# Optimization experiments

Measured on AMD Instinct MI355X. Metric: run time of the kernel, lower is better.

The kernel has to match this reference:

```python
import jax, jax.numpy as jnp
import numpy as np

MAX_LENGTH = 13
PAD_TOKEN = 0
HIDDEN = 1024
VOCAB = 32000
BATCH = 64


def gru_cell(x, h, w_ih, w_hh, b_ih, b_hh):
    # PyTorch GRU gate order: reset, update, new
    gi = x @ w_ih.T + b_ih            # [B, 3H]
    gh = h @ w_hh.T + b_hh            # [B, 3H]
    i_r, i_z, i_n = jnp.split(gi, 3, axis=-1)
    h_r, h_z, h_n = jnp.split(gh, 3, axis=-1)
    r = jax.nn.sigmoid(i_r + h_r)
    z = jax.nn.sigmoid(i_z + h_z)
    n = jnp.tanh(i_n + r * h_n)
    return (1.0 - z) * n + z * h


def setup_inputs() -> dict:
    key = jax.random.key(0)
    ks = jax.random.split(key, 9)
    s = 0.02
    return {
        "encoder_outputs": jax.random.normal(ks[0], (BATCH, MAX_LENGTH, HIDDEN), jnp.float32),
        "encoder_hidden": jax.random.normal(ks[1], (1, BATCH, HIDDEN), jnp.float32),
        "embedding": jax.random.normal(ks[2], (VOCAB, HIDDEN), jnp.float32) * s,
        "w_ih": jax.random.normal(ks[3], (3 * HIDDEN, HIDDEN), jnp.float32) * s,
        "w_hh": jax.random.normal(ks[4], (3 * HIDDEN, HIDDEN), jnp.float32) * s,
        "b_ih": jnp.zeros((3 * HIDDEN,), jnp.float32),
        "b_hh": jnp.zeros((3 * HIDDEN,), jnp.float32),
        "w_out": jax.random.normal(ks[5], (VOCAB, HIDDEN), jnp.float32) * s,
        "b_out": jnp.zeros((VOCAB,), jnp.float32),
    }


def reference(encoder_outputs, encoder_hidden, embedding, w_ih, w_hh, b_ih, b_hh, w_out, b_out):
    batch = encoder_outputs.shape[0]
    h0 = encoder_hidden[0]                               # [B, H]
    tok0 = jnp.full((batch,), PAD_TOKEN, dtype=jnp.int32)

    def step(carry, _):
        h, tok = carry
        x = jax.nn.relu(embedding[tok])                  # embed + relu
        h = gru_cell(x, h, w_ih, w_hh, b_ih, b_hh)       # GRU cell
        logits = h @ w_out.T + b_out                     # [B, V]
        nxt = jnp.argmax(logits, axis=-1).astype(jnp.int32)  # greedy feedback (topk(1))
        return (h, nxt), logits

    (h_final, _), logits = jax.lax.scan(step, (h0, tok0), None, length=MAX_LENGTH)
    logits = jnp.transpose(logits, (1, 0, 2))            # [B, T, V]
    log_probs = jax.nn.log_softmax(logits, axis=-1)
    return log_probs, h_final[None]
```

## Files before the change

### kernel.cpp

```cpp
#include <hip/hip_runtime.h>
#include <math.h>

#define BB 64
#define HH 1024
#define VV 32000
#define TT 13
#define QS 8000
#define BKL 128

typedef float f32x4 __attribute__((ext_vector_type(4)));
typedef __bf16 bf16x8 __attribute__((ext_vector_type(8)));

__device__ __forceinline__ unsigned short f2bf(float f) {
  unsigned u = __float_as_uint(f);
  u = (u + 0x7fffu + ((u >> 16) & 1u)) >> 16;
  return (unsigned short)u;
}
__device__ __forceinline__ float bf2f(unsigned short s) {
  return __uint_as_float(((unsigned)s) << 16);
}

__device__ __forceinline__ void gld16(const void* g, void* l) {
  __builtin_amdgcn_global_load_lds(
      (const __attribute__((address_space(1))) unsigned int*)g,
      (__attribute__((address_space(3))) unsigned int*)l, 16, 0, 0);
}

__global__ __launch_bounds__(1024) void k_init(
    const float* __restrict__ enc, const float* __restrict__ emb,
    float* __restrict__ hrm, unsigned short* __restrict__ hhi,
    unsigned short* __restrict__ hlo, unsigned short* __restrict__ xhi,
    unsigned short* __restrict__ xlo) {
  const int g = blockIdx.x * 1024 + threadIdx.x;
  const float h = enc[g];
  hrm[g] = h;
  const unsigned short h16 = f2bf(h);
  hhi[g] = h16;
  hlo[g] = f2bf(h - bf2f(h16));
  float e = emb[threadIdx.x];
  e = e > 0.f ? e : 0.f;
  const unsigned short e16 = f2bf(e);
  xhi[g] = e16;
  xlo[g] = f2bf(e - bf2f(e16));
}

__global__ __launch_bounds__(256) void k_wconv(const float* __restrict__ w,
                                               unsigned short* __restrict__ o) {
  const int n4 = VV * HH / 4;
  for (int i = blockIdx.x * 256 + threadIdx.x; i < n4; i += gridDim.x * 256) {
    const f32x4 v = ((const f32x4*)w)[i];
    ushort4 u;
    u.x = f2bf(v[0]); u.y = f2bf(v[1]); u.z = f2bf(v[2]); u.w = f2bf(v[3]);
    ((ushort4*)o)[i] = u;
  }
}

__global__ __launch_bounds__(256) void k_wconv2(
    const float* __restrict__ wih, const float* __restrict__ whh,
    unsigned short* __restrict__ ghi, unsigned short* __restrict__ glo) {
  const int n4 = 6 * HH * HH / 4;
  for (int i = blockIdx.x * 256 + threadIdx.x; i < n4; i += gridDim.x * 256) {
    const int flat = i * 4;
    const float* src = flat < 3 * HH * HH ? wih + flat : whh + (flat - 3 * HH * HH);
    const f32x4 v = *(const f32x4*)src;
    ushort4 hi, lo;
    hi.x = f2bf(v[0]); lo.x = f2bf(v[0] - bf2f(hi.x));
    hi.y = f2bf(v[1]); lo.y = f2bf(v[1] - bf2f(hi.y));
    hi.z = f2bf(v[2]); lo.z = f2bf(v[2] - bf2f(hi.z));
    hi.w = f2bf(v[3]); lo.w = f2bf(v[3] - bf2f(hi.w));
    ((ushort4*)ghi)[i] = hi;
    ((ushort4*)glo)[i] = lo;
  }
}

__global__ __launch_bounds__(64) void k_gru(
    const unsigned short* __restrict__ xhi, const unsigned short* __restrict__ xlo,
    const unsigned short* __restrict__ hhi_s, const unsigned short* __restrict__ hlo_s,
    const unsigned short* __restrict__ ghi, const unsigned short* __restrict__ glo,
    const float* __restrict__ wih, const float* __restrict__ whh,
    float* __restrict__ gbuf, int cachegw) {
  const int blk = blockIdx.x, lane = threadIdx.x;
  const int kh = blk & 1;
  const int r2 = blk >> 1;
  const int g6 = r2 % 6, jt = r2 / 6;
  const unsigned short* Ahi = g6 < 3 ? xhi : hhi_s;
  const unsigned short* Alo = g6 < 3 ? xlo : hlo_s;
  const int cl = lane & 15, kk = (lane >> 4) * 8;
  const int j = jt * 16 + cl;
  const int kbeg = kh * 512;
  f32x4 acc[4];
  acc[0] = acc[1] = acc[2] = acc[3] = (f32x4){0.f, 0.f, 0.f, 0.f};

  if (cachegw) {
    const unsigned short* bh = ghi + (size_t)(g6 * HH + j) * HH + kbeg;
    const unsigned short* bl = glo + (size_t)(g6 * HH + j) * HH + kbeg;
    const unsigned short* ah = Ahi + kbeg;
    const unsigned short* al = Alo + kbeg;
    #pragma unroll 4
    for (int k0 = 0; k0 < 512; k0 += 32) {
      const bf16x8 whi = *(const bf16x8*)(bh + k0 + kk);
      const bf16x8 wlo = *(const bf16x8*)(bl + k0 + kk);
      #pragma unroll
      for (int rt = 0; rt < 4; ++rt) {
        const size_t aoff = (size_t)(rt * 16 + cl) * HH + k0 + kk;
        const bf16x8 a_h = *(const bf16x8*)(ah + aoff);
        const bf16x8 a_l = *(const bf16x8*)(al + aoff);
        acc[rt] = __builtin_amdgcn_mfma_f32_16x16x32_bf16(a_h, whi, acc[rt], 0, 0, 0);
        acc[rt] = __builtin_amdgcn_mfma_f32_16x16x32_bf16(a_l, whi, acc[rt], 0, 0, 0);
        acc[rt] = __builtin_amdgcn_mfma_f32_16x16x32_bf16(a_h, wlo, acc[rt], 0, 0, 0);
      }
    }
  } else {
    const float* W = (g6 < 3 ? wih : whh) + (size_t)((g6 % 3) * HH + j) * HH + kbeg;
    for (int k0 = 0; k0 < 512; k0 += 32) {
      const f32x4 w0 = *(const f32x4*)(W + k0 + kk);
      const f32x4 w1 = *(const f32x4*)(W + k0 + kk + 4);
      union { unsigned short u[8]; bf16x8 b; } chi, clo;
      #pragma unroll
      for (int u2 = 0; u2 < 4; ++u2) {
        chi.u[u2] = f2bf(w0[u2]); clo.u[u2] = f2bf(w0[u2] - bf2f(chi.u[u2]));
        chi.u[4 + u2] = f2bf(w1[u2]); clo.u[4 + u2] = f2bf(w1[u2] - bf2f(chi.u[4 + u2]));
      }
      #pragma unroll
      for (int rt = 0; rt < 4; ++rt) {
        const size_t aoff = (size_t)(rt * 16 + cl) * HH + kbeg + k0 + kk;
        const bf16x8 a_h = *(const bf16x8*)(Ahi + aoff);
        const bf16x8 a_l = *(const bf16x8*)(Alo + aoff);
        acc[rt] = __builtin_amdgcn_mfma_f32_16x16x32_bf16(a_h, chi.b, acc[rt], 0, 0, 0);
        acc[rt] = __builtin_amdgcn_mfma_f32_16x16x32_bf16(a_l, chi.b, acc[rt], 0, 0, 0);
        acc[rt] = __builtin_amdgcn_mfma_f32_16x16x32_bf16(a_h, clo.b, acc[rt], 0, 0, 0);
      }
    }
  }
  #pragma unroll
  for (int rt = 0; rt < 4; ++rt)
    #pragma unroll
    for (int rg = 0; rg < 4; ++rg) {
      const int row = rt * 16 + (lane >> 4) * 4 + rg;
      gbuf[(size_t)((kh * 6 + g6) * BB + row) * HH + jt * 16 + cl] = acc[rt][rg];
    }
}

__global__ __launch_bounds__(256) void k_gep(
    const float* __restrict__ gbuf, const float* __restrict__ bih,
    const float* __restrict__ bhh, const float* __restrict__ hsrc,
    float* __restrict__ hdst, unsigned short* __restrict__ hhi_d,
    unsigned short* __restrict__ hlo_d) {
  const int e = blockIdx.x * 256 + threadIdx.x;
  const int b = e >> 10, j = e & (HH - 1);
  const size_t base = (size_t)b * HH + j;
  const float gir = gbuf[(size_t)(0 * BB + b) * HH + j] + gbuf[(size_t)((6 + 0) * BB + b) * HH + j] + bih[j];
  const float giz = gbuf[(size_t)(1 * BB + b) * HH + j] + gbuf[(size_t)((6 + 1) * BB + b) * HH + j] + bih[HH + j];
  const float gin = gbuf[(size_t)(2 * BB + b) * HH + j] + gbuf[(size_t)((6 + 2) * BB + b) * HH + j] + bih[2 * HH + j];
  const float ghr = gbuf[(size_t)(3 * BB + b) * HH + j] + gbuf[(size_t)((6 + 3) * BB + b) * HH + j] + bhh[j];
  const float ghz = gbuf[(size_t)(4 * BB + b) * HH + j] + gbuf[(size_t)((6 + 4) * BB + b) * HH + j] + bhh[HH + j];
  const float ghn = gbuf[(size_t)(5 * BB + b) * HH + j] + gbuf[(size_t)((6 + 5) * BB + b) * HH + j] + bhh[2 * HH + j];
  const float r_ = 1.f / (1.f + __expf(-(gir + ghr)));
  const float z_ = 1.f / (1.f + __expf(-(giz + ghz)));
  const float n_ = tanhf(gin + r_ * ghn);
  const float hnew = (1.f - z_) * n_ + z_ * hsrc[base];
  hdst[base] = hnew;
  const unsigned short h16 = f2bf(hnew);
  hhi_d[base] = h16;
  hlo_d[base] = f2bf(hnew - bf2f(h16));
}

__global__ __launch_bounds__(512, 1) void k_logits_lds(
    const unsigned short* __restrict__ hb,
    const unsigned short* __restrict__ wbf,
    const float* __restrict__ bout, float* __restrict__ lbuf) {
  __shared__ __attribute__((aligned(16))) unsigned char sA[2][64 * BKL * 2];
  __shared__ __attribute__((aligned(16))) unsigned char sB[2][128 * BKL * 2];
  const int tid = threadIdx.x, blk = blockIdx.x;
  const int lane = tid & 63, wv = tid >> 6;
  const int cl = lane & 15, kk = (lane >> 4) * 8;

  auto STAGE = [&](int buf, int k0) {
    #pragma unroll
    for (int it = 0; it < 2; ++it) {
      const int c = it * 512 + tid;
      const int r = c >> 4;
      const int kb = (c & 15) * 16;
      const int kbs = kb ^ ((r & 7) << 4);
      gld16(hb + (size_t)r * HH + k0 + (kbs >> 1),
            &sA[buf][it * 8192 + wv * 1024]);
    }
    #pragma unroll
    for (int it = 0; it < 4; ++it) {
      const int c = it * 512 + tid;
      const int col = c >> 4;
      const int kb = (c & 15) * 16;
      const int kbs = kb ^ ((col & 7) << 4);
      gld16(wbf + (size_t)(blk * 128 + col) * HH + k0 + (kbs >> 1),
            &sB[buf][it * 8192 + wv * 1024]);
    }
  };

  f32x4 acc[4];
  acc[0] = acc[1] = acc[2] = acc[3] = (f32x4){0.f, 0.f, 0.f, 0.f};

  STAGE(0, 0);
  for (int t = 0; t < HH / BKL; ++t) {
    const int cur = t & 1;
    if (t < HH / BKL - 1) {
      STAGE(cur ^ 1, (t + 1) * BKL);
      asm volatile("s_waitcnt vmcnt(6)" ::: "memory");
    } else {
      asm volatile("s_waitcnt vmcnt(0)" ::: "memory");
    }
    __builtin_amdgcn_s_barrier();
    __builtin_amdgcn_sched_barrier(0);
    #pragma unroll
    for (int ks = 0; ks < BKL; ks += 32) {
      const int bc = wv * 16 + cl;
      const bf16x8 bfr = *(const bf16x8*)&sB[cur][bc * (BKL * 2) + (((ks + kk) * 2) ^ ((bc & 7) << 4))];
      #pragma unroll
      for (int rt = 0; rt < 4; ++rt) {
        const int ar = rt * 16 + cl;
        const bf16x8 afr = *(const bf16x8*)&sA[cur][ar * (BKL * 2) + (((ks + kk) * 2) ^ ((ar & 7) << 4))];
        acc[rt] = __builtin_amdgcn_mfma_f32_16x16x32_bf16(afr, bfr, acc[rt], 0, 0, 0);
      }
    }
    __builtin_amdgcn_s_barrier();
    __builtin_amdgcn_sched_barrier(0);
  }

  const int col = blk * 128 + wv * 16 + cl;
  const float bo = bout[col];
  #pragma unroll
  for (int rt = 0; rt < 4; ++rt)
    #pragma unroll
    for (int rg = 0; rg < 4; ++rg) {
      const int row = rt * 16 + (lane >> 4) * 4 + rg;
      lbuf[(size_t)row * VV + col] = acc[rt][rg] + bo;
    }
}

__global__ __launch_bounds__(256) void k_logits_fb(
    const unsigned short* __restrict__ hb, const float* __restrict__ wout,
    const float* __restrict__ bout, float* __restrict__ lbuf) {
  const int tid = threadIdx.x, blk = blockIdx.x;
  const int lane = tid & 63, wv = tid >> 6;
  const int n0 = blk * 64 + wv * 16;
  const int cl = lane & 15, kk = (lane >> 4) * 8;
  f32x4 acc[4];
  acc[0] = acc[1] = acc[2] = acc[3] = (f32x4){0.f, 0.f, 0.f, 0.f};
  const float* wrow = wout + (size_t)(n0 + cl) * HH;
  for (int k0 = 0; k0 < HH; k0 += 32) {
    const f32x4 w0 = *(const f32x4*)(wrow + k0 + kk);
    const f32x4 w1 = *(const f32x4*)(wrow + k0 + kk + 4);
    union { unsigned short u[8]; bf16x8 b; } cv;
    #pragma unroll
    for (int u2 = 0; u2 < 4; ++u2) { cv.u[u2] = f2bf(w0[u2]); cv.u[4 + u2] = f2bf(w1[u2]); }
    #pragma unroll
    for (int rt = 0; rt < 4; ++rt) {
      const bf16x8 afr = *(const bf16x8*)(hb + (size_t)(rt * 16 + cl) * HH + k0 + kk);
      acc[rt] = __builtin_amdgcn_mfma_f32_16x16x32_bf16(afr, cv.b, acc[rt], 0, 0, 0);
    }
  }
  const int col = n0 + cl;
  const float bo = bout[col];
  #pragma unroll
  for (int rt = 0; rt < 4; ++rt)
    #pragma unroll
    for (int rg = 0; rg < 4; ++rg) {
      const int row = rt * 16 + (lane >> 4) * 4 + rg;
      lbuf[(size_t)row * VV + col] = acc[rt][rg] + bo;
    }
}

__global__ __launch_bounds__(256) void k_sum(
    const float* __restrict__ lbuf, const float* __restrict__ wout,
    const float* __restrict__ bout, const float* __restrict__ hnew,
    float* __restrict__ mq, float* __restrict__ sq,
    float* __restrict__ qbestV, int* __restrict__ qbestI, int dorecheck) {
  __shared__ float srow[QS];
  __shared__ float red[4];
  __shared__ int icnt;
  __shared__ int scand[32];
  const int tid = threadIdx.x;
  const int b = blockIdx.x >> 2, q = blockIdx.x & 3;
  const int lane = tid & 63, wv = tid >> 6;
  const f32x4* src = (const f32x4*)(lbuf + (size_t)b * VV + q * QS);
  f32x4* s4 = (f32x4*)srow;

  float m = -3.0e38f;
  for (int i = tid; i < QS / 4; i += 256) {
    const f32x4 v = src[i];
    s4[i] = v;
    m = fmaxf(fmaxf(fmaxf(m, v[0]), v[1]), fmaxf(v[2], v[3]));
  }
  #pragma unroll
  for (int d = 1; d < 64; d <<= 1) m = fmaxf(m, __shfl_xor(m, d, 64));
  if (lane == 0) red[wv] = m;
  if (tid == 0) icnt = 0;
  __syncthreads();
  const float M = fmaxf(fmaxf(red[0], red[1]), fmaxf(red[2], red[3]));

  float s = 0.f;
  for (int i = tid; i < QS / 4; i += 256) {
    const f32x4 v = s4[i];
    s += __expf(v[0] - M) + __expf(v[1] - M) + __expf(v[2] - M) + __expf(v[3] - M);
  }
  #pragma unroll
  for (int d = 1; d < 64; d <<= 1) s += __shfl_xor(s, d, 64);
  __syncthreads();
  if (lane == 0) red[wv] = s;
  __syncthreads();
  if (tid == 0) {
    mq[b * 4 + q] = M;
    sq[b * 4 + q] = red[0] + red[1] + red[2] + red[3];
  }

  if (dorecheck) {
    const float thr = M - 0.05f;
    for (int i = tid; i < QS / 4; i += 256) {
      const f32x4 v = s4[i];
      #pragma unroll
      for (int u = 0; u < 4; ++u)
        if (v[u] >= thr) {
          const int c = atomicAdd(&icnt, 1);
          if (c < 32) scand[c] = q * QS + 4 * i + u;
        }
    }
    __syncthreads();
    if (wv == 0) {
      const int nc = icnt < 32 ? icnt : 32;
      const float* hrow = hnew + (size_t)b * HH;
      f32x4 h4[4];
      #pragma unroll
      for (int u = 0; u < 4; ++u) h4[u] = *(const f32x4*)(hrow + lane * 16 + u * 4);
      float best = -3.0e38f; int bi = 0x7fffffff;
      for (int ci = 0; ci < nc; ++ci) {
        const int v = scand[ci];
        const float* wrow = wout + (size_t)v * HH + lane * 16;
        float ss = 0.f;
        #pragma unroll
        for (int u = 0; u < 4; ++u) {
          const f32x4 w4 = *(const f32x4*)(wrow + u * 4);
          ss += h4[u][0] * w4[0] + h4[u][1] * w4[1] + h4[u][2] * w4[2] + h4[u][3] * w4[3];
        }
        #pragma unroll
        for (int d = 1; d < 64; d <<= 1) ss += __shfl_xor(ss, d, 64);
        ss += bout[v];
        if (ss > best || (ss == best && v < bi)) { best = ss; bi = v; }
      }
      if (lane == 0) { qbestV[b * 4 + q] = best; qbestI[b * 4 + q] = bi; }
    }
  }
}

__global__ __launch_bounds__(256) void k_out(
    const float* __restrict__ lbuf, const float* __restrict__ mq,
    const float* __restrict__ sq, const float* __restrict__ qbestV,
    const int* __restrict__ qbestI, const float* __restrict__ emb,
    const float* __restrict__ hnew, float* __restrict__ out,
    unsigned short* __restrict__ xhi, unsigned short* __restrict__ xlo, int t) {
  __shared__ int stok;
  const int tid = threadIdx.x;
  const int b = blockIdx.x >> 2, q = blockIdx.x & 3;

  const float m0 = mq[b * 4 + 0], m1 = mq[b * 4 + 1];
  const float m2 = mq[b * 4 + 2], m3 = mq[b * 4 + 3];
  const float Mg = fmaxf(fmaxf(m0, m1), fmaxf(m2, m3));
  const float Sg = sq[b * 4 + 0] * __expf(m0 - Mg) + sq[b * 4 + 1] * __expf(m1 - Mg) +
                   sq[b * 4 + 2] * __expf(m2 - Mg) + sq[b * 4 + 3] * __expf(m3 - Mg);
  const float LZ = Mg + logf(Sg);

  const f32x4* src = (const f32x4*)(lbuf + (size_t)b * VV + q * QS);
  f32x4* dst = (f32x4*)(out + ((size_t)b * TT + t) * VV + q * QS);
  for (int i = tid; i < QS / 4; i += 256)
    dst[i] = src[i] - LZ;

  if (q == 0 && t < TT - 1) {
    if (tid == 0) {
      float bv = qbestV[b * 4 + 0]; int bi = qbestI[b * 4 + 0];
      #pragma unroll
      for (int qq = 1; qq < 4; ++qq) {
        const float v = qbestV[b * 4 + qq]; const int i2 = qbestI[b * 4 + qq];
        if (v > bv || (v == bv && i2 < bi)) { bv = v; bi = i2; }
      }
      stok = bi;
    }
    __syncthreads();
    const int tok = stok;
    for (int j = tid; j < HH; j += 256) {
      float e = emb[(size_t)tok * HH + j];
      e = e > 0.f ? e : 0.f;
      const unsigned short e16 = f2bf(e);
      xhi[(size_t)b * HH + j] = e16;
      xlo[(size_t)b * HH + j] = f2bf(e - bf2f(e16));
    }
  }
  if (q == 0 && t == TT - 1) {
    for (int j = tid; j < HH; j += 256)
      out[(size_t)BB * TT * VV + (size_t)b * HH + j] = hnew[(size_t)b * HH + j];
  }
}

extern "C" void kernel_launch(void* const* d_in, const int* in_sizes, int n_in,
                              void* d_out, int out_size, void* d_ws, size_t ws_size,
                              hipStream_t stream) {
  const float* enc  = (const float*)d_in[1];
  const float* emb  = (const float*)d_in[2];
  const float* wih  = (const float*)d_in[3];
  const float* whh  = (const float*)d_in[4];
  const float* bih  = (const float*)d_in[5];
  const float* bhh  = (const float*)d_in[6];
  const float* wout = (const float*)d_in[7];
  const float* bout = (const float*)d_in[8];
  float* out = (float*)d_out;

  char* ws = (char*)d_ws;
  size_t off = 0;
  auto alloc = [&](size_t bytes) -> char* {
    char* p = ws + off;
    off += (bytes + 255) & ~(size_t)255;
    return p;
  };
  float* hrm = (float*)alloc((size_t)2 * BB * HH * 4);
  unsigned short* hhi = (unsigned short*)alloc((size_t)2 * BB * HH * 2);
  unsigned short* hlo = (unsigned short*)alloc((size_t)2 * BB * HH * 2);
  unsigned short* xhi = (unsigned short*)alloc((size_t)BB * HH * 2);
  unsigned short* xlo = (unsigned short*)alloc((size_t)BB * HH * 2);
  float* gbuf = (float*)alloc((size_t)12 * BB * HH * 4);
  float* lbuf = (float*)alloc((size_t)BB * VV * 4);
  float* mq = (float*)alloc((size_t)BB * 4 * 4);
  float* sq = (float*)alloc((size_t)BB * 4 * 4);
  float* qbestV = (float*)alloc((size_t)BB * 4 * 4);
  int* qbestI = (int*)alloc((size_t)BB * 4 * 4);
  unsigned short* wbf = (unsigned short*)alloc((size_t)VV * HH * 2);
  const int cachew = (ws_size >= off) ? 1 : 0;
  unsigned short* ghi = (unsigned short*)alloc((size_t)6 * HH * HH * 2);
  unsigned short* glo = (unsigned short*)alloc((size_t)6 * HH * HH * 2);
  const int cachegw = (ws_size >= off) ? 1 : 0;

  hipLaunchKernelGGL(k_init, dim3(64), dim3(1024), 0, stream,
                     enc, emb, hrm, hhi, hlo, xhi, xlo);
  if (cachew)
    hipLaunchKernelGGL(k_wconv, dim3(2048), dim3(256), 0, stream, wout, wbf);
  if (cachegw)
    hipLaunchKernelGGL(k_wconv2, dim3(1024), dim3(256), 0, stream, wih, whh, ghi, glo);

  for (int t = 0; t < TT; ++t) {
    const int p = t & 1;
    const float* hsrc = hrm + (size_t)p * BB * HH;
    float* hdst = hrm + (size_t)(p ^ 1) * BB * HH;
    const unsigned short* hhs = hhi + (size_t)p * BB * HH;
    const unsigned short* hls = hlo + (size_t)p * BB * HH;
    unsigned short* hhd = hhi + (size_t)(p ^ 1) * BB * HH;
    unsigned short* hld = hlo + (size_t)(p ^ 1) * BB * HH;

    hipLaunchKernelGGL(k_gru, dim3(768), dim3(64), 0, stream,
                       xhi, xlo, hhs, hls, ghi, glo, wih, whh, gbuf, cachegw);
    hipLaunchKernelGGL(k_gep, dim3(256), dim3(256), 0, stream,
                       gbuf, bih, bhh, hsrc, hdst, hhd, hld);
    if (cachew)
      hipLaunchKernelGGL(k_logits_lds, dim3(250), dim3(512), 0, stream,
                         hhd, wbf, bout, lbuf);
    else
      hipLaunchKernelGGL(k_logits_fb, dim3(500), dim3(256), 0, stream,
                         hhd, wout, bout, lbuf);
    hipLaunchKernelGGL(k_sum, dim3(256), dim3(256), 0, stream,
                       lbuf, wout, bout, hdst, mq, sq, qbestV, qbestI,
                       (t < TT - 1) ? 1 : 0);
    hipLaunchKernelGGL(k_out, dim3(256), dim3(256), 0, stream,
                       lbuf, mq, sq, qbestV, qbestI, emb, hdst, out, xhi, xlo, t);
  }
}
```

Before: 927.0 us.

## Fuse GRU gemm with gate epilogue and merge per-step softmax/argmax kernels

Replaces the split-K GRU gemm plus separate gate-epilogue kernel with one kernel. Each block computes all six gate projections for 4 hidden columns across 6 waves over the full K, then applies the GRU nonlinearity from shared memory. It also merges the two-kernel log-softmax/argmax-recheck/output path into one 64-block, 1024-thread kernel per batch row. This cuts launches and the global gbuf round trip, but the GRU MFMAs now keep only 4 of 16 output columns, wasting 3/4 of the compute, and the reduction uses only 64 blocks.

New measurement: 1.538 ms. +65.9%, slower.

```diff
diff --git a/kernel.cpp b/kernel.cpp
--- a/kernel.cpp
+++ b/kernel.cpp
@@ -73,12 +73,245 @@
   }
 }
 
-__global__ __launch_bounds__(64) void k_gru(
+__global__ __launch_bounds__(384, 1) void k_gruE(
     const unsigned short* __restrict__ xhi, const unsigned short* __restrict__ xlo,
     const unsigned short* __restrict__ hhi_s, const unsigned short* __restrict__ hlo_s,
     const unsigned short* __restrict__ ghi, const unsigned short* __restrict__ glo,
+    const float* __restrict__ bih, const float* __restrict__ bhh,
+    const float* __restrict__ hsrc, float* __restrict__ hdst,
+    unsigned short* __restrict__ hhi_d, unsigned short* __restrict__ hlo_d) {
+  __shared__ float g[6][64][9];
+  const int blk = blockIdx.x, tid = threadIdx.x;
+  const int lane = tid & 63, wv = tid >> 6;
+  const int cl = lane & 15, kk = (lane >> 4) * 8;
+  {
+    const int g6 = wv;
+    const unsigned short* Ahi = g6 < 3 ? xhi : hhi_s;
+    const unsigned short* Alo = g6 < 3 ? xlo : hlo_s;
+    const int col = blk * 4 + (cl & 3);
+    const unsigned short* bh = ghi + (size_t)(g6 * HH + col) * HH;
+    const unsigned short* bl = glo + (size_t)(g6 * HH + col) * HH;
+    f32x4 acc[4];
+    acc[0] = acc[1] = acc[2] = acc[3] = (f32x4){0.f, 0.f, 0.f, 0.f};
+    #pragma unroll 4
+    for (int k0 = 0; k0 < HH; k0 += 32) {
+      const bf16x8 whi = *(const bf16x8*)(bh + k0 + kk);
+      const bf16x8 wlo = *(const bf16x8*)(bl + k0 + kk);
+      #pragma unroll
+      for (int rt = 0; rt < 4; ++rt) {
+        const size_t aoff = (size_t)(rt * 16 + cl) * HH + k0 + kk;
+        const bf16x8 a_h = *(const bf16x8*)(Ahi + aoff);
+        const bf16x8 a_l = *(const bf16x8*)(Alo + aoff);
+        acc[rt] = __builtin_amdgcn_mfma_f32_16x16x32_bf16(a_h, whi, acc[rt], 0, 0, 0);
+        acc[rt] = __builtin_amdgcn_mfma_f32_16x16x32_bf16(a_l, whi, acc[rt], 0, 0, 0);
+        acc[rt] = __builtin_amdgcn_mfma_f32_16x16x32_bf16(a_h, wlo, acc[rt], 0, 0, 0);
+      }
+    }
+    if (cl < 4) {
+      #pragma unroll
+      for (int rt = 0; rt < 4; ++rt)
+        #pragma unroll
+        for (int rg = 0; rg < 4; ++rg)
+          g[g6][rt * 16 + (lane >> 4) * 4 + rg][cl] = acc[rt][rg];
+    }
+  }
+  __syncthreads();
+  if (tid < 256) {
+    const int c = tid & 3, b = tid >> 2;
+    const int j = blk * 4 + c;
+    const size_t base = (size_t)b * HH + j;
+    const float gir = g[0][b][c] + bih[j];
+    const float giz = g[1][b][c] + bih[HH + j];
+    const float gin = g[2][b][c] + bih[2 * HH + j];
+    const float ghr = g[3][b][c] + bhh[j];
+    const float ghz = g[4][b][c] + bhh[HH + j];
+    const float ghn = g[5][b][c] + bhh[2 * HH + j];
+    const float r_ = 1.f / (1.f + __expf(-(gir + ghr)));
+    const float z_ = 1.f / (1.f + __expf(-(giz + ghz)));
+    const float n_ = tanhf(gin + r_ * ghn);
+    const float hnew = (1.f - z_) * n_ + z_ * hsrc[base];
+    hdst[base] = hnew;
+    const unsigned short h16 = f2bf(hnew);
+    hhi_d[base] = h16;
+    hlo_d[base] = f2bf(hnew - bf2f(h16));
+  }
+}
+
+__global__ __launch_bounds__(512, 1) void k_logits_lds(
+    const unsigned short* __restrict__ hb,
+    const unsigned short* __restrict__ wbf,
+    const float* __restrict__ bout, float* __restrict__ lbuf) {
+  __shared__ __attribute__((aligned(16))) unsigned char sA[2][64 * BKL * 2];
+  __shared__ __attribute__((aligned(16))) unsigned char sB[2][128 * BKL * 2];
+  const int tid = threadIdx.x, blk = blockIdx.x;
+  const int lane = tid & 63, wv = tid >> 6;
+  const int cl = lane & 15, kk = (lane >> 4) * 8;
+
+  auto STAGE = [&](int buf, int k0) {
+    #pragma unroll
+    for (int it = 0; it < 2; ++it) {
+      const int c = it * 512 + tid;
+      const int r = c >> 4;
+      const int kb = (c & 15) * 16;
+      const int kbs = kb ^ ((r & 7) << 4);
+      gld16(hb + (size_t)r * HH + k0 + (kbs >> 1),
+            &sA[buf][it * 8192 + wv * 1024]);
+    }
+    #pragma unroll
+    for (int it = 0; it < 4; ++it) {
+      const int c = it * 512 + tid;
+      const int col = c >> 4;
+      const int kb = (c & 15) * 16;
+      const int kbs = kb ^ ((col & 7) << 4);
+      gld16(wbf + (size_t)(blk * 128 + col) * HH + k0 + (kbs >> 1),
+            &sB[buf][it * 8192 + wv * 1024]);
+    }
+  };
+
+  f32x4 acc[4];
+  acc[0] = acc[1] = acc[2] = acc[3] = (f32x4){0.f, 0.f, 0.f, 0.f};
+
+  STAGE(0, 0);
+  for (int t = 0; t < HH / BKL; ++t) {
+    const int cur = t & 1;
+    if (t < HH / BKL - 1) {
+      STAGE(cur ^ 1, (t + 1) * BKL);
+      asm volatile("s_waitcnt vmcnt(6)" ::: "memory");
+    } else {
+      asm volatile("s_waitcnt vmcnt(0)" ::: "memory");
+    }
+    __builtin_amdgcn_s_barrier();
+    __builtin_amdgcn_sched_barrier(0);
+    #pragma unroll
+    for (int ks = 0; ks < BKL; ks += 32) {
+      const int bc = wv * 16 + cl;
+      const bf16x8 bfr = *(const bf16x8*)&sB[cur][bc * (BKL * 2) + (((ks + kk) * 2) ^ ((bc & 7) << 4))];
+      #pragma unroll
+      for (int rt = 0; rt < 4; ++rt) {
+        const int ar = rt * 16 + cl;
+        const bf16x8 afr = *(const bf16x8*)&sA[cur][ar * (BKL * 2) + (((ks + kk) * 2) ^ ((ar & 7) << 4))];
+        acc[rt] = __builtin_amdgcn_mfma_f32_16x16x32_bf16(afr, bfr, acc[rt], 0, 0, 0);
+      }
+    }
+    __builtin_amdgcn_s_barrier();
+    __builtin_amdgcn_sched_barrier(0);
+  }
+
+  const int col = blk * 128 + wv * 16 + cl;
+  const float bo = bout[col];
+  #pragma unroll
+  for (int rt = 0; rt < 4; ++rt)
+    #pragma unroll
+    for (int rg = 0; rg < 4; ++rg) {
+      const int row = rt * 16 + (lane >> 4) * 4 + rg;
+      lbuf[(size_t)row * VV + col] = acc[rt][rg] + bo;
+    }
+}
+
+__global__ __launch_bounds__(1024, 1) void k_red(
+    const float* __restrict__ lbuf, const float* __restrict__ wout,
+    const float* __restrict__ bout, const float* __restrict__ emb,
+    const float* __restrict__ hnew, float* __restrict__ out,
+    unsigned short* __restrict__ xhi, unsigned short* __restrict__ xlo, int t) {
+  __shared__ struct {
+    float srow[VV];
+    float red[16];
+    int icnt, stok;
+    int scand[64];
+  } sm;
+  const int tid = threadIdx.x, b = blockIdx.x;
+  const int lane = tid & 63, wv = tid >> 6;
+  const f32x4* src = (const f32x4*)(lbuf + (size_t)b * VV);
+  f32x4* s4 = (f32x4*)sm.srow;
+
+  float m = -3.0e38f;
+  for (int i = tid; i < VV / 4; i += 1024) {
+    const f32x4 v = src[i];
+    s4[i] = v;
+    m = fmaxf(fmaxf(fmaxf(m, v[0]), v[1]), fmaxf(v[2], v[3]));
+  }
+  #pragma unroll
+  for (int d = 1; d < 64; d <<= 1) m = fmaxf(m, __shfl_xor(m, d, 64));
+  if (lane == 0) sm.red[wv] = m;
+  if (tid == 0) sm.icnt = 0;
+  __syncthreads();
+  float M = sm.red[0];
+  #pragma unroll
+  for (int w = 1; w < 16; ++w) M = fmaxf(M, sm.red[w]);
+
+  float s = 0.f;
+  for (int i = tid; i < VV / 4; i += 1024) {
+    const f32x4 v = s4[i];
+    s += __expf(v[0] - M) + __expf(v[1] - M) + __expf(v[2] - M) + __expf(v[3] - M);
+  }
+  #pragma unroll
+  for (int d = 1; d < 64; d <<= 1) s += __shfl_xor(s, d, 64);
+  __syncthreads();
+  if (lane == 0) sm.red[wv] = s;
+  __syncthreads();
+  float S = sm.red[0];
+  #pragma unroll
+  for (int w = 1; w < 16; ++w) S += sm.red[w];
+  const float LZ = M + logf(S);
+
+  if (t < TT - 1) {
+    const float thr = M - 0.05f;
+    for (int i = tid; i < VV / 4; i += 1024) {
+      const f32x4 v = s4[i];
+      #pragma unroll
+      for (int u = 0; u < 4; ++u)
+        if (v[u] >= thr) {
+          const int c = atomicAdd(&sm.icnt, 1);
+          if (c < 64) sm.scand[c] = 4 * i + u;
+        }
+    }
+    __syncthreads();
+    if (wv == 0) {
+      const int nc = sm.icnt < 64 ? sm.icnt : 64;
+      const float* hrow = hnew + (size_t)b * HH;
+      f32x4 h4[4];
+      #pragma unroll
+      for (int u = 0; u < 4; ++u) h4[u] = *(const f32x4*)(hrow + lane * 16 + u * 4);
+      float best = -3.0e38f; int bi = 0x7fffffff;
+      for (int ci = 0; ci < nc; ++ci) {
+        const int v = sm.scand[ci];
+        const float* wrow = wout + (size_t)v * HH + lane * 16;
+        float ss = 0.f;
+        #pragma unroll
+        for (int u = 0; u < 4; ++u) {
+          const f32x4 w4 = *(const f32x4*)(wrow + u * 4);
+          ss += h4[u][0] * w4[0] + h4[u][1] * w4[1] + h4[u][2] * w4[2] + h4[u][3] * w4[3];
+        }
+        #pragma unroll
+        for (int d = 1; d < 64; d <<= 1) ss += __shfl_xor(ss, d, 64);
+        ss += bout[v];
+        if (ss > best || (ss == best && v < bi)) { best = ss; bi = v; }
+      }
+      if (lane == 0) sm.stok = bi;
+    }
+    __syncthreads();
+    const int tok = sm.stok;
+    {
+      float e = emb[(size_t)tok * HH + tid];
+      e = e > 0.f ? e : 0.f;
+      const unsigned short e16 = f2bf(e);
+      xhi[(size_t)b * HH + tid] = e16;
+      xlo[(size_t)b * HH + tid] = f2bf(e - bf2f(e16));
+    }
+  }
+
+  f32x4* dst = (f32x4*)(out + ((size_t)b * TT + t) * VV);
+  for (int i = tid; i < VV / 4; i += 1024)
+    dst[i] = s4[i] - LZ;
+  if (t == TT - 1)
+    out[(size_t)BB * TT * VV + (size_t)b * HH + tid] = hnew[(size_t)b * HH + tid];
+}
+
+__global__ __launch_bounds__(64) void k_gru_fb(
+    const unsigned short* __restrict__ xhi, const unsigned short* __restrict__ xlo,
+    const unsigned short* __restrict__ hhi_s, const unsigned short* __restrict__ hlo_s,
     const float* __restrict__ wih, const float* __restrict__ whh,
-    float* __restrict__ gbuf, int cachegw) {
+    float* __restrict__ gbuf) {
   const int blk = blockIdx.x, lane = threadIdx.x;
   const int kh = blk & 1;
   const int r2 = blk >> 1;
@@ -90,46 +323,24 @@
   const int kbeg = kh * 512;
   f32x4 acc[4];
   acc[0] = acc[1] = acc[2] = acc[3] = (f32x4){0.f, 0.f, 0.f, 0.f};
-
-  if (cachegw) {
-    const unsigned short* bh = ghi + (size_t)(g6 * HH + j) * HH + kbeg;
-    const unsigned short* bl = glo + (size_t)(g6 * HH + j) * HH + kbeg;
-    const unsigned short* ah = Ahi + kbeg;
-    const unsigned short* al = Alo + kbeg;
-    #pragma unroll 4
-    for (int k0 = 0; k0 < 512; k0 += 32) {
-      const bf16x8 whi = *(const bf16x8*)(bh + k0 + kk);
-      const bf16x8 wlo = *(const bf16x8*)(bl + k0 + kk);
-      #pragma unroll
-      for (int rt = 0; rt < 4; ++rt) {
-        const size_t aoff = (size_t)(rt * 16 + cl) * HH + k0 + kk;
-        const bf16x8 a_h = *(const bf16x8*)(ah + aoff);
-        const bf16x8 a_l = *(const bf16x8*)(al + aoff);
-        acc[rt] = __builtin_amdgcn_mfma_f32_16x16x32_bf16(a_h, whi, acc[rt], 0, 0, 0);
-        acc[rt] = __builtin_amdgcn_mfma_f32_16x16x32_bf16(a_l, whi, acc[rt], 0, 0, 0);
-        acc[rt] = __builtin_amdgcn_mfma_f32_16x16x32_bf16(a_h, wlo, acc[rt], 0, 0, 0);
-      }
-    }
-  } else {
-    const float* W = (g6 < 3 ? wih : whh) + (size_t)((g6 % 3) * HH + j) * HH + kbeg;
-    for (int k0 = 0; k0 < 512; k0 += 32) {
-      const f32x4 w0 = *(const f32x4*)(W + k0 + kk);
-      const f32x4 w1 = *(const f32x4*)(W + k0 + kk + 4);
-      union { unsigned short u[8]; bf16x8 b; } chi, clo;
-      #pragma unroll
-      for (int u2 = 0; u2 < 4; ++u2) {
-        chi.u[u2] = f2bf(w0[u2]); clo.u[u2] = f2bf(w0[u2] - bf2f(chi.u[u2]));
-        chi.u[4 + u2] = f2bf(w1[u2]); clo.u[4 + u2] = f2bf(w1[u2] - bf2f(chi.u[4 + u2]));
-      }
-      #pragma unroll
-      for (int rt = 0; rt < 4; ++rt) {
-        const size_t aoff = (size_t)(rt * 16 + cl) * HH + kbeg + k0 + kk;
-        const bf16x8 a_h = *(const bf16x8*)(Ahi + aoff);
-        const bf16x8 a_l = *(const bf16x8*)(Alo + aoff);
-        acc[rt] = __builtin_amdgcn_mfma_f32_16x16x32_bf16(a_h, chi.b, acc[rt], 0, 0, 0);
-        acc[rt] = __builtin_amdgcn_mfma_f32_16x16x32_bf16(a_l, chi.b, acc[rt], 0, 0, 0);
-        acc[rt] = __builtin_amdgcn_mfma_f32_16x16x32_bf16(a_h, clo.b, acc[rt], 0, 0, 0);
-      }
+  const float* W = (g6 < 3 ? wih : whh) + (size_t)((g6 % 3) * HH + j) * HH + kbeg;
+  for (int k0 = 0; k0 < 512; k0 += 32) {
+    const f32x4 w0 = *(const f32x4*)(W + k0 + kk);
+    const f32x4 w1 = *(const f32x4*)(W + k0 + kk + 4);
+    union { unsigned short u[8]; bf16x8 b; } chi, clo;
+    #pragma unroll
+    for (int u2 = 0; u2 < 4; ++u2) {
+      chi.u[u2] = f2bf(w0[u2]); clo.u[u2] = f2bf(w0[u2] - bf2f(chi.u[u2]));
+      chi.u[4 + u2] = f2bf(w1[u2]); clo.u[4 + u2] = f2bf(w1[u2] - bf2f(chi.u[4 + u2]));
+    }
+    #pragma unroll
+    for (int rt = 0; rt < 4; ++rt) {
+      const size_t aoff = (size_t)(rt * 16 + cl) * HH + kbeg + k0 + kk;
+      const bf16x8 a_h = *(const bf16x8*)(Ahi + aoff);
+      const bf16x8 a_l = *(const bf16x8*)(Alo + aoff);
+      acc[rt] = __builtin_amdgcn_mfma_f32_16x16x32_bf16(a_h, chi.b, acc[rt], 0, 0, 0);
+      acc[rt] = __builtin_amdgcn_mfma_f32_16x16x32_bf16(a_l, chi.b, acc[rt], 0, 0, 0);
+      acc[rt] = __builtin_amdgcn_mfma_f32_16x16x32_bf16(a_h, clo.b, acc[rt], 0, 0, 0);
     }
   }
   #pragma unroll
@@ -165,77 +376,6 @@
   hlo_d[base] = f2bf(hnew - bf2f(h16));
 }
 
-__global__ __launch_bounds__(512, 1) void k_logits_lds(
-    const unsigned short* __restrict__ hb,
-    const unsigned short* __restrict__ wbf,
-    const float* __restrict__ bout, float* __restrict__ lbuf) {
-  __shared__ __attribute__((aligned(16))) unsigned char sA[2][64 * BKL * 2];
-  __shared__ __attribute__((aligned(16))) unsigned char sB[2][128 * BKL * 2];
-  const int tid = threadIdx.x, blk = blockIdx.x;
-  const int lane = tid & 63, wv = tid >> 6;
-  const int cl = lane & 15, kk = (lane >> 4) * 8;
-
-  auto STAGE = [&](int buf, int k0) {
-    #pragma unroll
-    for (int it = 0; it < 2; ++it) {
-      const int c = it * 512 + tid;
-      const int r = c >> 4;
-      const int kb = (c & 15) * 16;
-      const int kbs = kb ^ ((r & 7) << 4);
-      gld16(hb + (size_t)r * HH + k0 + (kbs >> 1),
-            &sA[buf][it * 8192 + wv * 1024]);
-    }
-    #pragma unroll
-    for (int it = 0; it < 4; ++it) {
-      const int c = it * 512 + tid;
-      const int col = c >> 4;
-      const int kb = (c & 15) * 16;
-      const int kbs = kb ^ ((col & 7) << 4);
-      gld16(wbf + (size_t)(blk * 128 + col) * HH + k0 + (kbs >> 1),
-            &sB[buf][it * 8192 + wv * 1024]);
-    }
-  };
-
-  f32x4 acc[4];
-  acc[0] = acc[1] = acc[2] = acc[3] = (f32x4){0.f, 0.f, 0.f, 0.f};
-
-  STAGE(0, 0);
-  for (int t = 0; t < HH / BKL; ++t) {
-    const int cur = t & 1;
-    if (t < HH / BKL - 1) {
-      STAGE(cur ^ 1, (t + 1) * BKL);
-      asm volatile("s_waitcnt vmcnt(6)" ::: "memory");
-    } else {
-      asm volatile("s_waitcnt vmcnt(0)" ::: "memory");
-    }
-    __builtin_amdgcn_s_barrier();
-    __builtin_amdgcn_sched_barrier(0);
-    #pragma unroll
-    for (int ks = 0; ks < BKL; ks += 32) {
-      const int bc = wv * 16 + cl;
-      const bf16x8 bfr = *(const bf16x8*)&sB[cur][bc * (BKL * 2) + (((ks + kk) * 2) ^ ((bc & 7) << 4))];
-      #pragma unroll
-      for (int rt = 0; rt < 4; ++rt) {
-        const int ar = rt * 16 + cl;
-        const bf16x8 afr = *(const bf16x8*)&sA[cur][ar * (BKL * 2) + (((ks + kk) * 2) ^ ((ar & 7) << 4))];
-        acc[rt] = __builtin_amdgcn_mfma_f32_16x16x32_bf16(afr, bfr, acc[rt], 0, 0, 0);
-      }
-    }
-    __builtin_amdgcn_s_barrier();
-    __builtin_amdgcn_sched_barrier(0);
-  }
-
-  const int col = blk * 128 + wv * 16 + cl;
-  const float bo = bout[col];
-  #pragma unroll
-  for (int rt = 0; rt < 4; ++rt)
-    #pragma unroll
-    for (int rg = 0; rg < 4; ++rg) {
-      const int row = rt * 16 + (lane >> 4) * 4 + rg;
-      lbuf[(size_t)row * VV + col] = acc[rt][rg] + bo;
-    }
-}
-
 __global__ __launch_bounds__(256) void k_logits_fb(
     const unsigned short* __restrict__ hb, const float* __restrict__ wout,
     const float* __restrict__ bout, float* __restrict__ lbuf) {
@@ -269,135 +409,6 @@
     }
 }
 
-__global__ __launch_bounds__(256) void k_sum(
-    const float* __restrict__ lbuf, const float* __restrict__ wout,
-    const float* __restrict__ bout, const float* __restrict__ hnew,
-    float* __restrict__ mq, float* __restrict__ sq,
-    float* __restrict__ qbestV, int* __restrict__ qbestI, int dorecheck) {
-  __shared__ float srow[QS];
-  __shared__ float red[4];
-  __shared__ int icnt;
-  __shared__ int scand[32];
-  const int tid = threadIdx.x;
-  const int b = blockIdx.x >> 2, q = blockIdx.x & 3;
-  const int lane = tid & 63, wv = tid >> 6;
-  const f32x4* src = (const f32x4*)(lbuf + (size_t)b * VV + q * QS);
-  f32x4* s4 = (f32x4*)srow;
-
-  float m = -3.0e38f;
-  for (int i = tid; i < QS / 4; i += 256) {
-    const f32x4 v = src[i];
-    s4[i] = v;
-    m = fmaxf(fmaxf(fmaxf(m, v[0]), v[1]), fmaxf(v[2], v[3]));
-  }
-  #pragma unroll
-  for (int d = 1; d < 64; d <<= 1) m = fmaxf(m, __shfl_xor(m, d, 64));
-  if (lane == 0) red[wv] = m;
-  if (tid == 0) icnt = 0;
-  __syncthreads();
-  const float M = fmaxf(fmaxf(red[0], red[1]), fmaxf(red[2], red[3]));
-
-  float s = 0.f;
-  for (int i = tid; i < QS / 4; i += 256) {
-    const f32x4 v = s4[i];
-    s += __expf(v[0] - M) + __expf(v[1] - M) + __expf(v[2] - M) + __expf(v[3] - M);
-  }
-  #pragma unroll
-  for (int d = 1; d < 64; d <<= 1) s += __shfl_xor(s, d, 64);
-  __syncthreads();
-  if (lane == 0) red[wv] = s;
-  __syncthreads();
-  if (tid == 0) {
-    mq[b * 4 + q] = M;
-    sq[b * 4 + q] = red[0] + red[1] + red[2] + red[3];
-  }
-
-  if (dorecheck) {
-    const float thr = M - 0.05f;
-    for (int i = tid; i < QS / 4; i += 256) {
-      const f32x4 v = s4[i];
-      #pragma unroll
-      for (int u = 0; u < 4; ++u)
-        if (v[u] >= thr) {
-          const int c = atomicAdd(&icnt, 1);
-          if (c < 32) scand[c] = q * QS + 4 * i + u;
-        }
-    }
-    __syncthreads();
-    if (wv == 0) {
-      const int nc = icnt < 32 ? icnt : 32;
-      const float* hrow = hnew + (size_t)b * HH;
-      f32x4 h4[4];
-      #pragma unroll
-      for (int u = 0; u < 4; ++u) h4[u] = *(const f32x4*)(hrow + lane * 16 + u * 4);
-      float best = -3.0e38f; int bi = 0x7fffffff;
-      for (int ci = 0; ci < nc; ++ci) {
-        const int v = scand[ci];
-        const float* wrow = wout + (size_t)v * HH + lane * 16;
-        float ss = 0.f;
-        #pragma unroll
-        for (int u = 0; u < 4; ++u) {
-          const f32x4 w4 = *(const f32x4*)(wrow + u * 4);
-          ss += h4[u][0] * w4[0] + h4[u][1] * w4[1] + h4[u][2] * w4[2] + h4[u][3] * w4[3];
-        }
-        #pragma unroll
-        for (int d = 1; d < 64; d <<= 1) ss += __shfl_xor(ss, d, 64);
-        ss += bout[v];
-        if (ss > best || (ss == best && v < bi)) { best = ss; bi = v; }
-      }
-      if (lane == 0) { qbestV[b * 4 + q] = best; qbestI[b * 4 + q] = bi; }
-    }
-  }
-}
-
-__global__ __launch_bounds__(256) void k_out(
-    const float* __restrict__ lbuf, const float* __restrict__ mq,
-    const float* __restrict__ sq, const float* __restrict__ qbestV,
-    const int* __restrict__ qbestI, const float* __restrict__ emb,
-    const float* __restrict__ hnew, float* __restrict__ out,
-    unsigned short* __restrict__ xhi, unsigned short* __restrict__ xlo, int t) {
-  __shared__ int stok;
-  const int tid = threadIdx.x;
-  const int b = blockIdx.x >> 2, q = blockIdx.x & 3;
-
-  const float m0 = mq[b * 4 + 0], m1 = mq[b * 4 + 1];
-  const float m2 = mq[b * 4 + 2], m3 = mq[b * 4 + 3];
-  const float Mg = fmaxf(fmaxf(m0, m1), fmaxf(m2, m3));
-  const float Sg = sq[b * 4 + 0] * __expf(m0 - Mg) + sq[b * 4 + 1] * __expf(m1 - Mg) +
-                   sq[b * 4 + 2] * __expf(m2 - Mg) + sq[b * 4 + 3] * __expf(m3 - Mg);
-  const float LZ = Mg + logf(Sg);
-
-  const f32x4* src = (const f32x4*)(lbuf + (size_t)b * VV + q * QS);
-  f32x4* dst = (f32x4*)(out + ((size_t)b * TT + t) * VV + q * QS);
-  for (int i = tid; i < QS / 4; i += 256)
-    dst[i] = src[i] - LZ;
-
-  if (q == 0 && t < TT - 1) {
-    if (tid == 0) {
-      float bv = qbestV[b * 4 + 0]; int bi = qbestI[b * 4 + 0];
-      #pragma unroll
-      for (int qq = 1; qq < 4; ++qq) {
-        const float v = qbestV[b * 4 + qq]; const int i2 = qbestI[b * 4 + qq];
-        if (v > bv || (v == bv && i2 < bi)) { bv = v; bi = i2; }
-      }
-      stok = bi;
-    }
-    __syncthreads();
-    const int tok = stok;
-    for (int j = tid; j < HH; j += 256) {
-      float e = emb[(size_t)tok * HH + j];
-      e = e > 0.f ? e : 0.f;
-      const unsigned short e16 = f2bf(e);
-      xhi[(size_t)b * HH + j] = e16;
-      xlo[(size_t)b * HH + j] = f2bf(e - bf2f(e16));
-    }
-  }
-  if (q == 0 && t == TT - 1) {
-    for (int j = tid; j < HH; j += 256)
-      out[(size_t)BB * TT * VV + (size_t)b * HH + j] = hnew[(size_t)b * HH + j];
-  }
-}
-
 extern "C" void kernel_launch(void* const* d_in, const int* in_sizes, int n_in,
                               void* d_out, int out_size, void* d_ws, size_t ws_size,
                               hipStream_t stream) {
@@ -425,22 +436,17 @@
   unsigned short* xlo = (unsigned short*)alloc((size_t)BB * HH * 2);
   float* gbuf = (float*)alloc((size_t)12 * BB * HH * 4);
   float* lbuf = (float*)alloc((size_t)BB * VV * 4);
-  float* mq = (float*)alloc((size_t)BB * 4 * 4);
-  float* sq = (float*)alloc((size_t)BB * 4 * 4);
-  float* qbestV = (float*)alloc((size_t)BB * 4 * 4);
-  int* qbestI = (int*)alloc((size_t)BB * 4 * 4);
   unsigned short* wbf = (unsigned short*)alloc((size_t)VV * HH * 2);
-  const int cachew = (ws_size >= off) ? 1 : 0;
   unsigned short* ghi = (unsigned short*)alloc((size_t)6 * HH * HH * 2);
   unsigned short* glo = (unsigned short*)alloc((size_t)6 * HH * HH * 2);
-  const int cachegw = (ws_size >= off) ? 1 : 0;
+  const int cache_ok = (ws_size >= off) ? 1 : 0;
 
   hipLaunchKernelGGL(k_init, dim3(64), dim3(1024), 0, stream,
                      enc, emb, hrm, hhi, hlo, xhi, xlo);
-  if (cachew)
+  if (cache_ok) {
     hipLaunchKernelGGL(k_wconv, dim3(2048), dim3(256), 0, stream, wout, wbf);
-  if (cachegw)
     hipLaunchKernelGGL(k_wconv2, dim3(1024), dim3(256), 0, stream, wih, whh, ghi, glo);
+  }
 
   for (int t = 0; t < TT; ++t) {
     const int p = t & 1;
@@ -451,20 +457,21 @@
     unsigned short* hhd = hhi + (size_t)(p ^ 1) * BB * HH;
     unsigned short* hld = hlo + (size_t)(p ^ 1) * BB * HH;
 
-    hipLaunchKernelGGL(k_gru, dim3(768), dim3(64), 0, stream,
-                       xhi, xlo, hhs, hls, ghi, glo, wih, whh, gbuf, cachegw);
-    hipLaunchKernelGGL(k_gep, dim3(256), dim3(256), 0, stream,
-                       gbuf, bih, bhh, hsrc, hdst, hhd, hld);
-    if (cachew)
+    if (cache_ok) {
+      hipLaunchKernelGGL(k_gruE, dim3(256), dim3(384), 0, stream,
+                         xhi, xlo, hhs, hls, ghi, glo, bih, bhh,
+                         hsrc, hdst, hhd, hld);
       hipLaunchKernelGGL(k_logits_lds, dim3(250), dim3(512), 0, stream,
                          hhd, wbf, bout, lbuf);
-    else
+    } else {
+      hipLaunchKernelGGL(k_gru_fb, dim3(768), dim3(64), 0, stream,
+                         xhi, xlo, hhs, hls, wih, whh, gbuf);
+      hipLaunchKernelGGL(k_gep, dim3(256), dim3(256), 0, stream,
+                         gbuf, bih, bhh, hsrc, hdst, hhd, hld);
       hipLaunchKernelGGL(k_logits_fb, dim3(500), dim3(256), 0, stream,
                          hhd, wout, bout, lbuf);
-    hipLaunchKernelGGL(k_sum, dim3(256), dim3(256), 0, stream,
-                       lbuf, wout, bout, hdst, mq, sq, qbestV, qbestI,
-                       (t < TT - 1) ? 1 : 0);
-    hipLaunchKernelGGL(k_out, dim3(256), dim3(256), 0, stream,
-                       lbuf, mq, sq, qbestV, qbestI, emb, hdst, out, xhi, xlo, t);
-  }
-}
+    }
+    hipLaunchKernelGGL(k_red, dim3(64), dim3(1024), 0, stream,
+                       lbuf, wout, bout, emb, hdst, out, xhi, xlo, t);
+  }
+}
```
